# Performance work log

Hardware: AMD Instinct MI355X
Metric: run time of the kernel (lower is better)

Reference implementation:

```python
import jax, jax.numpy as jnp
from jax import lax
import numpy as np

DIM = 256


def setup_inputs() -> dict:
    key = jax.random.key(0)
    ks = jax.random.split(key, 7)
    B, C, H, W = 16, DIM, 64, 64
    s = 0.02
    return {
        "x": jax.random.normal(ks[0], (B, C, H, W), dtype=jnp.float32),
        "qkv_w": jax.random.normal(ks[1], (3 * C, C), dtype=jnp.float32) * s,
        "qkv_b": jnp.zeros((3 * C,), dtype=jnp.float32),
        "proj_w": jax.random.normal(ks[2], (C, C), dtype=jnp.float32) * s,
        "proj_b": jnp.zeros((C,), dtype=jnp.float32),
        "conv_w": jax.random.normal(ks[3], (C, C, 3, 3), dtype=jnp.float32) * s,
        "conv_b": jnp.zeros((C,), dtype=jnp.float32),
    }


def reference(x, qkv_w, qkv_b, proj_w, proj_b, conv_w, conv_b):
    B, C, H, W = x.shape
    N = H * W
    scale = C ** (-0.5)
    # qkv on channels-last tokens: [B,N,3C]
    xp = x.transpose(0, 2, 3, 1).reshape(B, N, C)
    qkv = xp @ qkv_w.T + qkv_b
    q, k, v = jnp.split(qkv, 3, axis=-1)  # each [B,N,C]
    q = q.transpose(0, 2, 1)  # [B,C,N]
    v = v.transpose(0, 2, 1)  # [B,C,N]
    # channel attention: [B,C,C]
    attn = jax.nn.softmax(jnp.einsum('bcn,bnd->bcd', q, k) * scale, axis=-1)
    out = jnp.einsum('bcd,bdn->bcn', attn, v).transpose(0, 2, 1)  # [B,N,C]
    out = out @ proj_w.T + proj_b  # [B,N,C]
    # faithful to original: direct reshape [B,N,C] -> [B,C,H,W]
    attn_out = out.reshape(B, C, H, W)
    conv_out = lax.conv_general_dilated(
        x, conv_w, window_strides=(1, 1), padding=[(1, 1), (1, 1)],
        dimension_numbers=('NCHW', 'OIHW', 'NCHW'))
    conv_out = conv_out + conv_b[None, :, None, None]
    return attn_out + conv_out
```

## Files before the change

kernel.cpp:

```cpp
#include <hip/hip_runtime.h>
#include <hip/hip_bf16.h>

typedef unsigned short u16;
typedef __bf16 bf16x8 __attribute__((ext_vector_type(8)));
typedef float f32x4 __attribute__((ext_vector_type(4)));

#define BATCH 16
#define C 256
#define NTOK 4096
#define CN 1048576

__device__ __forceinline__ u16 f2b(float f) {
  __hip_bfloat16 h = __float2bfloat16(f);
  return __builtin_bit_cast(u16, h);
}
__device__ __forceinline__ float b2f(u16 u) {
  unsigned int x = ((unsigned int)u) << 16;
  return __builtin_bit_cast(float, x);
}

__device__ __forceinline__ void glds16(const u16* g, u16* l) {
  __builtin_amdgcn_global_load_lds(
      (const __attribute__((address_space(1))) unsigned int*)(g),
      (__attribute__((address_space(3))) unsigned int*)(l), 16, 0, 0);
}

__global__ __launch_bounds__(256) void prep_x_kernel(
    const float* __restrict__ x, u16* __restrict__ xbf, u16* __restrict__ xT,
    float* __restrict__ rws) {
  __shared__ float t[32][33];
  int b = blockIdx.z;
  int c0 = blockIdx.y * 32, n0 = blockIdx.x * 32;
  int tid = threadIdx.x;
  int i = tid >> 3, j4 = (tid & 7) * 4;
  const float* xb = x + (long)b * CN;
  float4 v = *(const float4*)(xb + (long)(c0 + i) * NTOK + n0 + j4);
  ushort4 bv;
  bv.x = f2b(v.x); bv.y = f2b(v.y); bv.z = f2b(v.z); bv.w = f2b(v.w);
  *(ushort4*)(xbf + (long)b * CN + (long)(c0 + i) * NTOK + n0 + j4) = bv;
  t[i][j4 + 0] = v.x; t[i][j4 + 1] = v.y; t[i][j4 + 2] = v.z; t[i][j4 + 3] = v.w;
  __syncthreads();
  ushort4 o;
  o.x = f2b(t[j4 + 0][i]); o.y = f2b(t[j4 + 1][i]);
  o.z = f2b(t[j4 + 2][i]); o.w = f2b(t[j4 + 3][i]);
  *(ushort4*)(xT + (long)b * CN + (long)(n0 + i) * C + c0 + j4) = o;
  if (tid < 32) {
    float s = 0.f;
#pragma unroll
    for (int j = 0; j < 32; ++j) s += t[tid][j];
    atomicAdd(&rws[b * C + c0 + tid], s);
  }
}

__global__ __launch_bounds__(256) void prep_w_kernel(
    const float* __restrict__ qkv_w, const float* __restrict__ proj_w,
    const float* __restrict__ conv_w, u16* __restrict__ Wq, u16* __restrict__ Wk,
    u16* __restrict__ WvT, u16* __restrict__ Pw, u16* __restrict__ cw,
    float* __restrict__ rws, u16* __restrict__ zbuf) {
  int idx = blockIdx.x * 256 + threadIdx.x;
  if (idx < 4096) rws[idx] = 0.f;
  if (idx < 256) zbuf[idx] = 0;
  if (idx < 65536) {
    Wq[idx] = f2b(qkv_w[idx]);
  } else if (idx < 131072) {
    int e = idx - 65536;
    Wk[e] = f2b(qkv_w[65536 + e]);
  } else if (idx < 196608) {
    int e = idx - 131072;
    int i = e >> 8, d = e & 255;
    WvT[e] = f2b(qkv_w[131072 + d * 256 + i]);
  } else if (idx < 262144) {
    int e = idx - 196608;
    Pw[e] = f2b(proj_w[e]);
  } else if (idx < 851968) {
    int e = idx - 262144;
    int o = e / 2304;
    int rem = e - o * 2304;
    int tap = rem >> 8, i = rem & 255;
    cw[e] = f2b(conv_w[o * 2304 + i * 9 + tap]);
  }
}

__global__ __launch_bounds__(512) void bias_uw_kernel(
    const float* __restrict__ qkv_w, const float* __restrict__ r,
    float* __restrict__ u, float* __restrict__ w) {
  int b = blockIdx.x, t = threadIdx.x;
  const float* rb = r + b * C;
  if (t < 256) {
    float s = 0.f;
    for (int i = 0; i < C; ++i) s += qkv_w[(256 + t) * 256 + i] * rb[i];
    u[b * C + t] = s;
  } else {
    int c = t - 256;
    float s = 0.f;
    for (int i = 0; i < C; ++i) s += qkv_w[c * 256 + i] * rb[i];
    w[b * C + c] = s;
  }
}

template <int EPI>
__global__ __launch_bounds__(256, 2) void gemm_glds_kernel(
    const u16* __restrict__ A, const u16* __restrict__ B, void* __restrict__ Cv,
    int K, int lda, int ldb, int ldc, int tilesN, long sA, long sB, long sC,
    float scale, const float* __restrict__ e1, const float* __restrict__ e2,
    const float* __restrict__ e3, const float* __restrict__ e4, int e34stride) {
  int b = blockIdx.z, ks = blockIdx.y;
  A += (long)b * sA + (long)ks * K;
  B += (long)b * sB + (long)ks * K;
  int ty = blockIdx.x / tilesN, tx = blockIdx.x % tilesN;
  int row0 = ty * 128, col0 = tx * 128;

  __shared__ u16 lA[2][4096];
  __shared__ u16 lB[2][4096];

  int tid = threadIdx.x;
  int lane = tid & 63, wv = tid >> 6;
  int wm = wv >> 1, wn = wv & 1;
  int fr = lane & 15, kq = lane >> 4;
  int kqs = kq ^ ((fr >> 1) & 3);

  int c0 = wv * 128 + lane, c1 = c0 + 64;
  int r0s = c0 >> 2, r1s = c1 >> 2;
  int ls0 = (c0 & 3) ^ ((r0s >> 1) & 3);
  int ls1 = (c1 & 3) ^ ((r1s >> 1) & 3);
  const u16* pA0 = A + (long)(row0 + r0s) * lda + ls0 * 8;
  const u16* pA1 = A + (long)(row0 + r1s) * lda + ls1 * 8;
  const u16* pB0 = B + (long)(col0 + r0s) * ldb + ls0 * 8;
  const u16* pB1 = B + (long)(col0 + r1s) * ldb + ls1 * 8;
  int dst0 = wv * 1024, dst1 = wv * 1024 + 512;

  f32x4 acc[4][4] = {};

  auto STAGE = [&](int buf, int t) {
    int k0 = t << 5;
    glds16(pA0 + k0, &lA[buf][dst0]);
    glds16(pA1 + k0, &lA[buf][dst1]);
    glds16(pB0 + k0, &lB[buf][dst0]);
    glds16(pB1 + k0, &lB[buf][dst1]);
  };
  auto COMPUTE = [&](int buf) {
    bf16x8 af[4], bfr[4];
#pragma unroll
    for (int m = 0; m < 4; ++m)
      af[m] = *(const bf16x8*)&lA[buf][(wm * 64 + m * 16 + fr) * 32 + kqs * 8];
#pragma unroll
    for (int n = 0; n < 4; ++n)
      bfr[n] = *(const bf16x8*)&lB[buf][(wn * 64 + n * 16 + fr) * 32 + kqs * 8];
#pragma unroll
    for (int m = 0; m < 4; ++m)
#pragma unroll
      for (int n = 0; n < 4; ++n)
        acc[m][n] = __builtin_amdgcn_mfma_f32_16x16x32_bf16(af[m], bfr[n], acc[m][n], 0, 0, 0);
  };

  int nk = K >> 5, cur = 0;
  STAGE(0, 0);
  __syncthreads();
  for (int t = 0; t < nk; ++t) {
    if (t + 1 < nk) STAGE(cur ^ 1, t + 1);
    COMPUTE(cur);
    __syncthreads();
    cur ^= 1;
  }

  if (EPI == 0) {
    float* Cb = (float*)Cv + ((long)b * gridDim.y + ks) * sC;
#pragma unroll
    for (int m = 0; m < 4; ++m)
#pragma unroll
      for (int n = 0; n < 4; ++n)
#pragma unroll
        for (int r = 0; r < 4; ++r) {
          int gr = row0 + wm * 64 + m * 16 + kq * 4 + r;
          int gc = col0 + wn * 64 + n * 16 + fr;
          Cb[(long)gr * ldc + gc] = acc[m][n][r];
        }
  } else if (EPI == 1) {
    __hip_bfloat16* Cb = (__hip_bfloat16*)Cv + (long)b * sC;
#pragma unroll
    for (int m = 0; m < 4; ++m)
#pragma unroll
      for (int n = 0; n < 4; ++n)
#pragma unroll
        for (int r = 0; r < 4; ++r) {
          int gr = row0 + wm * 64 + m * 16 + kq * 4 + r;
          int gc = col0 + wn * 64 + n * 16 + fr;
          Cb[(long)gr * ldc + gc] = __float2bfloat16(acc[m][n][r]);
        }
  } else if (EPI == 2) {
    float* Cb = (float*)Cv + (long)b * sC;
    const float* ub = e3 + (long)b * e34stride;
    const float* wb = e4 + (long)b * e34stride;
#pragma unroll
    for (int m = 0; m < 4; ++m)
#pragma unroll
      for (int n = 0; n < 4; ++n)
#pragma unroll
        for (int r = 0; r < 4; ++r) {
          int gr = row0 + wm * 64 + m * 16 + kq * 4 + r;
          int gc = col0 + wn * 64 + n * 16 + fr;
          float v = acc[m][n][r] + e1[gr] * ub[gc] + e2[gc] * wb[gr] +
                    4096.0f * e1[gr] * e2[gc];
          Cb[(long)gr * ldc + gc] = v * scale;
        }
  }
}

__global__ __launch_bounds__(256) void reduceG_kernel(
    const float* __restrict__ Gp, u16* __restrict__ G) {
  int b = blockIdx.y;
  int e = blockIdx.x * 1024 + threadIdx.x * 4;
  const float* base = Gp + (long)b * 262144;
  float4 s = *(const float4*)(base + e);
#pragma unroll
  for (int sl = 1; sl < 4; ++sl) {
    float4 v = *(const float4*)(base + sl * 65536 + e);
    s.x += v.x; s.y += v.y; s.z += v.z; s.w += v.w;
  }
  ushort4 o;
  o.x = f2b(s.x); o.y = f2b(s.y); o.z = f2b(s.z); o.w = f2b(s.w);
  *(ushort4*)(G + (long)b * 65536 + e) = o;
}

__global__ __launch_bounds__(256) void softmax_kernel(const float* __restrict__ S,
                                                      u16* __restrict__ attnT) {
  int row = blockIdx.x;
  int t = threadIdx.x;
  float v = S[(long)row * C + t];
  __shared__ float red[256];
  red[t] = v; __syncthreads();
  for (int st = 128; st > 0; st >>= 1) {
    if (t < st) red[t] = fmaxf(red[t], red[t + st]);
    __syncthreads();
  }
  float mx = red[0];
  __syncthreads();
  float e = __expf(v - mx);
  red[t] = e; __syncthreads();
  for (int st = 128; st > 0; st >>= 1) {
    if (t < st) red[t] += red[t + st];
    __syncthreads();
  }
  float inv = 1.0f / red[0];
  int b = row >> 8, c = row & 255;
  attnT[(long)b * 65536 + t * 256 + c] = f2b(e * inv);
}

__global__ __launch_bounds__(256) void cbias_kernel(const u16* __restrict__ M,
                                                    const float* __restrict__ qkv_b,
                                                    const float* __restrict__ proj_b,
                                                    float* __restrict__ cb) {
  int b = blockIdx.x, j = threadIdx.x;
  const u16* m = M + (long)b * 65536 + (long)j * 256;
  float s = 0.f;
  for (int d = 0; d < C; ++d) s += b2f(m[d]) * qkv_b[512 + d];
  cb[b * C + j] = proj_b[j] + s;
}

__global__ __launch_bounds__(256, 2) void convattn_kernel(
    const u16* __restrict__ xT, const u16* __restrict__ cw,
    const u16* __restrict__ W2, const u16* __restrict__ zbuf,
    const float* __restrict__ conv_b, const float* __restrict__ cb,
    float* __restrict__ out) {
  int b = blockIdx.y;
  int to = blockIdx.x >> 5;
  int tn = blockIdx.x & 31;
  int row0 = to * 128, col0 = tn * 128;
  const u16* xTb = xT + (long)b * CN;
  const u16* W2b = W2 + (long)b * 65536;

  __shared__ u16 lA[2][8192];
  __shared__ u16 lB[2][8192];

  int tid = threadIdx.x;
  int lane = tid & 63, w = tid >> 6;
  int wm = w >> 1, wn = w & 1;
  int fr = lane & 15, kq = lane >> 4;
  int fx = fr & 7;

  int lr = lane >> 3, sl = lane & 7;
  int ss = sl ^ lr;

  const u16* aA[4]; const u16* pBt[4]; int hh[4], ww[4];
  const u16* zsrc = zbuf + ss * 8;
#pragma unroll
  for (int i = 0; i < 4; ++i) {
    int r = w * 32 + i * 8 + lr;
    aA[i] = cw + (long)(row0 + r) * 2304 + ss * 8;
    int t = col0 + r;
    hh[i] = t >> 6; ww[i] = t & 63;
    pBt[i] = xTb + (long)t * 256 + ss * 8;
  }
  int nb = col0 >> 8, jb = col0 & 255;

  f32x4 acc[4][4] = {};
  const u16 *at0, *at1, *at2, *at3, *bt0, *bt1, *bt2, *bt3;

  auto set_tap = [&](int tap) {
    int dh = tap / 3 - 1, dw = tap % 3 - 1;
    long sh = (long)(dh * 64 + dw) * 256;
    at0 = aA[0] + tap * 256; at1 = aA[1] + tap * 256;
    at2 = aA[2] + tap * 256; at3 = aA[3] + tap * 256;
    bool v0 = ((unsigned)(hh[0] + dh) < 64u) && ((unsigned)(ww[0] + dw) < 64u);
    bool v1 = ((unsigned)(hh[1] + dh) < 64u) && ((unsigned)(ww[1] + dw) < 64u);
    bool v2 = ((unsigned)(hh[2] + dh) < 64u) && ((unsigned)(ww[2] + dw) < 64u);
    bool v3 = ((unsigned)(hh[3] + dh) < 64u) && ((unsigned)(ww[3] + dw) < 64u);
    bt0 = v0 ? pBt[0] + sh : zsrc;
    bt1 = v1 ? pBt[1] + sh : zsrc;
    bt2 = v2 ? pBt[2] + sh : zsrc;
    bt3 = v3 ? pBt[3] + sh : zsrc;
  };
  auto set_attn = [&]() {
#pragma unroll
    for (int i = 0; i < 4; ++i) {
      int r = w * 32 + i * 8 + lr;
      const u16* a = xTb + (long)((row0 + r) * 16 + nb) * 256 + ss * 8;
      const u16* bb = W2b + (long)(jb + r) * 256 + ss * 8;
      if (i == 0) { at0 = a; bt0 = bb; }
      else if (i == 1) { at1 = a; bt1 = bb; }
      else if (i == 2) { at2 = a; bt2 = bb; }
      else { at3 = a; bt3 = bb; }
    }
  };

  auto STAGE = [&](int buf, int chunk) {
    int k = chunk * 64;
    glds16(at0 + k, &lA[buf][(w * 32 + 0) * 64]);
    glds16(at1 + k, &lA[buf][(w * 32 + 8) * 64]);
    glds16(at2 + k, &lA[buf][(w * 32 + 16) * 64]);
    glds16(at3 + k, &lA[buf][(w * 32 + 24) * 64]);
    glds16(bt0 + k, &lB[buf][(w * 32 + 0) * 64]);
    glds16(bt1 + k, &lB[buf][(w * 32 + 8) * 64]);
    glds16(bt2 + k, &lB[buf][(w * 32 + 16) * 64]);
    glds16(bt3 + k, &lB[buf][(w * 32 + 24) * 64]);
  };
  auto COMPUTE = [&](int buf) {
    bf16x8 af[4][2], bf[4][2];
#pragma unroll
    for (int m = 0; m < 4; ++m) {
      int row = wm * 64 + m * 16 + fr;
#pragma unroll
      for (int kh = 0; kh < 2; ++kh)
        af[m][kh] = *(const bf16x8*)&lA[buf][row * 64 + (((kh << 2) + kq) ^ fx) * 8];
    }
#pragma unroll
    for (int n = 0; n < 4; ++n) {
      int row = wn * 64 + n * 16 + fr;
#pragma unroll
      for (int kh = 0; kh < 2; ++kh)
        bf[n][kh] = *(const bf16x8*)&lB[buf][row * 64 + (((kh << 2) + kq) ^ fx) * 8];
    }
    __builtin_amdgcn_s_setprio(1);
#pragma unroll
    for (int kh = 0; kh < 2; ++kh)
#pragma unroll
      for (int m = 0; m < 4; ++m)
#pragma unroll
        for (int n = 0; n < 4; ++n)
          acc[m][n] = __builtin_amdgcn_mfma_f32_16x16x32_bf16(af[m][kh], bf[n][kh], acc[m][n], 0, 0, 0);
    __builtin_amdgcn_s_setprio(0);
  };

  set_tap(0);
  STAGE(0, 0);
  asm volatile("s_waitcnt vmcnt(0)" ::: "memory");
  __builtin_amdgcn_sched_barrier(0);
  __builtin_amdgcn_s_barrier();
  __builtin_amdgcn_sched_barrier(0);

  int buf = 0;
#pragma unroll 1
  for (int T = 0; T < 10; ++T) {
#pragma unroll
    for (int j = 0; j < 4; ++j) {
      if (!(T == 9 && j == 3)) {
        if (j < 3) {
          STAGE(buf ^ 1, j + 1);
        } else {
          if (T < 8) set_tap(T + 1);
          else set_attn();
          STAGE(buf ^ 1, 0);
        }
      }
      COMPUTE(buf);
      asm volatile("s_waitcnt vmcnt(0)" ::: "memory");
      __builtin_amdgcn_sched_barrier(0);
      __builtin_amdgcn_s_barrier();
      __builtin_amdgcn_sched_barrier(0);
      buf ^= 1;
    }
  }

  float* ob = out + (long)b * CN;
  const float* cbb = cb + b * C;
#pragma unroll
  for (int m = 0; m < 4; ++m) {
    int go = row0 + wm * 64 + m * 16 + kq * 4;
#pragma unroll
    for (int nn = 0; nn < 4; ++nn) {
      int cc = wn * 64 + nn * 16 + fr;
      float cbv = cbb[jb + cc];
#pragma unroll
      for (int r = 0; r < 4; ++r)
        ob[(long)(go + r) * NTOK + col0 + cc] =
            acc[m][nn][r] + conv_b[go + r] + cbv;
    }
  }
}

extern "C" void kernel_launch(void* const* d_in, const int* in_sizes, int n_in,
                              void* d_out, int out_size, void* d_ws, size_t ws_size,
                              hipStream_t stream) {
  const float* x = (const float*)d_in[0];
  const float* qkv_w = (const float*)d_in[1];
  const float* qkv_b = (const float*)d_in[2];
  const float* proj_w = (const float*)d_in[3];
  const float* proj_b = (const float*)d_in[4];
  const float* conv_w = (const float*)d_in[5];
  const float* conv_b = (const float*)d_in[6];
  float* out = (float*)d_out;
  char* ws = (char*)d_ws;

  u16* xbf = (u16*)(ws);
  u16* xT = (u16*)(ws + 33554432);
  u16* Gbf = (u16*)(ws + 67108864);
  float* Gpart = (float*)(ws + 69206016);
  u16* T1bf = (u16*)(ws + 69206016);
  float* Sf = (float*)(ws + 71303168);
  u16* attnT = (u16*)(ws + 75497472);
  u16* Mbf = (u16*)(ws + 77594624);
  u16* W2bf = (u16*)(ws + 79691776);
  u16* Wq = (u16*)(ws + 85983232);
  u16* Wk = (u16*)(ws + 86114304);
  u16* WvT = (u16*)(ws + 86245376);
  u16* Pw = (u16*)(ws + 86376448);
  u16* cw = (u16*)(ws + 86507520);
  float* rws = (float*)(ws + 87687168);
  float* uws = (float*)(ws + 87703552);
  float* wws = (float*)(ws + 87719936);
  float* cb = (float*)(ws + 87736320);
  u16* zbuf = (u16*)(ws + 87752704);

  prep_w_kernel<<<3328, 256, 0, stream>>>(qkv_w, proj_w, conv_w, Wq, Wk, WvT,
                                          Pw, cw, rws, zbuf);
  prep_x_kernel<<<dim3(128, 8, BATCH), 256, 0, stream>>>(x, xbf, xT, rws);
  bias_uw_kernel<<<BATCH, 512, 0, stream>>>(qkv_w, rws, uws, wws);

  gemm_glds_kernel<0><<<dim3(4, 4, BATCH), 256, 0, stream>>>(
      xbf, xbf, Gpart, 1024, 4096, 4096, 256, 2, CN, CN, 65536,
      0.f, nullptr, nullptr, nullptr, nullptr, 0);
  reduceG_kernel<<<dim3(64, BATCH), 256, 0, stream>>>(Gpart, Gbf);

  gemm_glds_kernel<1><<<dim3(4, 1, BATCH), 256, 0, stream>>>(
      Wq, Gbf, T1bf, 256, 256, 256, 256, 2, 0, 65536, 65536,
      0.f, nullptr, nullptr, nullptr, nullptr, 0);
  gemm_glds_kernel<2><<<dim3(4, 1, BATCH), 256, 0, stream>>>(
      T1bf, Wk, Sf, 256, 256, 256, 256, 2, 65536, 0, 65536,
      0.0625f, qkv_b, qkv_b + 256, uws, wws, 256);

  softmax_kernel<<<BATCH * C, 256, 0, stream>>>(Sf, attnT);

  gemm_glds_kernel<1><<<dim3(4, 1, BATCH), 256, 0, stream>>>(
      Pw, attnT, Mbf, 256, 256, 256, 256, 2, 0, 65536, 65536,
      0.f, nullptr, nullptr, nullptr, nullptr, 0);
  cbias_kernel<<<BATCH, 256, 0, stream>>>(Mbf, qkv_b, proj_b, cb);
  gemm_glds_kernel<1><<<dim3(4, 1, BATCH), 256, 0, stream>>>(
      Mbf, WvT, W2bf, 256, 256, 256, 256, 2, 65536, 0, 65536,
      0.f, nullptr, nullptr, nullptr, nullptr, 0);

  convattn_kernel<<<dim3(64, BATCH), 256, 0, stream>>>(xT, cw, W2bf, zbuf,
                                                       conv_b, cb, out);
}
```

Baseline: 218.6 us.

## Load A operand directly from global into registers, dropping A LDS staging

The conv-weight and attention A-operand tiles are now read by each lane straight from global memory into double-buffered registers in MFMA fragment layout, instead of being staged through shared memory. This halves LDS use and removes the A-side LDS reads, which could raise occupancy and cut LDS traffic. In exchange each wave issues uncoalesced 16-byte global loads, and rows shared by two waves (wn=0/1) are fetched twice. Register pressure also grows from the two A register buffers.

```diff
diff --git a/kernel.cpp b/kernel.cpp
--- a/kernel.cpp
+++ b/kernel.cpp
@@ -269,7 +269,6 @@
   const u16* xTb = xT + (long)b * CN;
   const u16* W2b = W2 + (long)b * 65536;
 
-  __shared__ u16 lA[2][8192];
   __shared__ u16 lB[2][8192];
 
   int tid = threadIdx.x;
@@ -281,26 +280,31 @@
   int lr = lane >> 3, sl = lane & 7;
   int ss = sl ^ lr;
 
-  const u16* aA[4]; const u16* pBt[4]; int hh[4], ww[4];
+  const u16* pBt[4]; int hh[4], ww[4];
   const u16* zsrc = zbuf + ss * 8;
 #pragma unroll
   for (int i = 0; i < 4; ++i) {
-    int r = w * 32 + i * 8 + lr;
-    aA[i] = cw + (long)(row0 + r) * 2304 + ss * 8;
-    int t = col0 + r;
+    int t = col0 + w * 32 + i * 8 + lr;
     hh[i] = t >> 6; ww[i] = t & 63;
     pBt[i] = xTb + (long)t * 256 + ss * 8;
   }
   int nb = col0 >> 8, jb = col0 & 255;
 
+  const u16* aP[4];
+#pragma unroll
+  for (int m = 0; m < 4; ++m)
+    aP[m] = cw + (long)(row0 + wm * 64 + m * 16 + fr) * 2304 + kq * 8;
+  const u16* aQ[4];
+#pragma unroll
+  for (int m = 0; m < 4; ++m)
+    aQ[m] = xTb + (long)((row0 + wm * 64 + m * 16 + fr) * 16 + nb) * 256 + kq * 8;
+
   f32x4 acc[4][4] = {};
-  const u16 *at0, *at1, *at2, *at3, *bt0, *bt1, *bt2, *bt3;
-
-  auto set_tap = [&](int tap) {
+  const u16 *bt0, *bt1, *bt2, *bt3;
+
+  auto set_tapB = [&](int tap) {
     int dh = tap / 3 - 1, dw = tap % 3 - 1;
     long sh = (long)(dh * 64 + dw) * 256;
-    at0 = aA[0] + tap * 256; at1 = aA[1] + tap * 256;
-    at2 = aA[2] + tap * 256; at3 = aA[3] + tap * 256;
     bool v0 = ((unsigned)(hh[0] + dh) < 64u) && ((unsigned)(ww[0] + dw) < 64u);
     bool v1 = ((unsigned)(hh[1] + dh) < 64u) && ((unsigned)(ww[1] + dw) < 64u);
     bool v2 = ((unsigned)(hh[2] + dh) < 64u) && ((unsigned)(ww[2] + dw) < 64u);
@@ -310,45 +314,39 @@
     bt2 = v2 ? pBt[2] + sh : zsrc;
     bt3 = v3 ? pBt[3] + sh : zsrc;
   };
-  auto set_attn = [&]() {
-#pragma unroll
-    for (int i = 0; i < 4; ++i) {
-      int r = w * 32 + i * 8 + lr;
-      const u16* a = xTb + (long)((row0 + r) * 16 + nb) * 256 + ss * 8;
-      const u16* bb = W2b + (long)(jb + r) * 256 + ss * 8;
-      if (i == 0) { at0 = a; bt0 = bb; }
-      else if (i == 1) { at1 = a; bt1 = bb; }
-      else if (i == 2) { at2 = a; bt2 = bb; }
-      else { at3 = a; bt3 = bb; }
-    }
-  };
-
-  auto STAGE = [&](int buf, int chunk) {
+  auto set_attnB = [&]() {
+    bt0 = W2b + (long)(jb + w * 32 + 0 + lr) * 256 + ss * 8;
+    bt1 = W2b + (long)(jb + w * 32 + 8 + lr) * 256 + ss * 8;
+    bt2 = W2b + (long)(jb + w * 32 + 16 + lr) * 256 + ss * 8;
+    bt3 = W2b + (long)(jb + w * 32 + 24 + lr) * 256 + ss * 8;
+  };
+
+  auto STAGE_B = [&](int buf, int chunk) {
     int k = chunk * 64;
-    glds16(at0 + k, &lA[buf][(w * 32 + 0) * 64]);
-    glds16(at1 + k, &lA[buf][(w * 32 + 8) * 64]);
-    glds16(at2 + k, &lA[buf][(w * 32 + 16) * 64]);
-    glds16(at3 + k, &lA[buf][(w * 32 + 24) * 64]);
     glds16(bt0 + k, &lB[buf][(w * 32 + 0) * 64]);
     glds16(bt1 + k, &lB[buf][(w * 32 + 8) * 64]);
     glds16(bt2 + k, &lB[buf][(w * 32 + 16) * 64]);
     glds16(bt3 + k, &lB[buf][(w * 32 + 24) * 64]);
   };
-  auto COMPUTE = [&](int buf) {
-    bf16x8 af[4][2], bf[4][2];
+
+  bf16x8 aR0[4][2], aR1[4][2];
+  auto LOADA = [&](bf16x8 (&d)[4][2]) {
 #pragma unroll
     for (int m = 0; m < 4; ++m) {
-      int row = wm * 64 + m * 16 + fr;
-#pragma unroll
-      for (int kh = 0; kh < 2; ++kh)
-        af[m][kh] = *(const bf16x8*)&lA[buf][row * 64 + (((kh << 2) + kq) ^ fx) * 8];
+      d[m][0] = *(const bf16x8*)(aP[m]);
+      d[m][1] = *(const bf16x8*)(aP[m] + 32);
     }
+#pragma unroll
+    for (int m = 0; m < 4; ++m) aP[m] += 64;
+  };
+  auto COMPUTE = [&](int buf, const bf16x8 (&a)[4][2]) {
+    bf16x8 bf_[4][2];
 #pragma unroll
     for (int n = 0; n < 4; ++n) {
       int row = wn * 64 + n * 16 + fr;
 #pragma unroll
       for (int kh = 0; kh < 2; ++kh)
-        bf[n][kh] = *(const bf16x8*)&lB[buf][row * 64 + (((kh << 2) + kq) ^ fx) * 8];
+        bf_[n][kh] = *(const bf16x8*)&lB[buf][row * 64 + (((kh << 2) + kq) ^ fx) * 8];
     }
     __builtin_amdgcn_s_setprio(1);
 #pragma unroll
@@ -357,12 +355,13 @@
       for (int m = 0; m < 4; ++m)
 #pragma unroll
         for (int n = 0; n < 4; ++n)
-          acc[m][n] = __builtin_amdgcn_mfma_f32_16x16x32_bf16(af[m][kh], bf[n][kh], acc[m][n], 0, 0, 0);
+          acc[m][n] = __builtin_amdgcn_mfma_f32_16x16x32_bf16(a[m][kh], bf_[n][kh], acc[m][n], 0, 0, 0);
     __builtin_amdgcn_s_setprio(0);
   };
 
-  set_tap(0);
-  STAGE(0, 0);
+  set_tapB(0);
+  STAGE_B(0, 0);
+  LOADA(aR0);
   asm volatile("s_waitcnt vmcnt(0)" ::: "memory");
   __builtin_amdgcn_sched_barrier(0);
   __builtin_amdgcn_s_barrier();
@@ -373,16 +372,20 @@
   for (int T = 0; T < 10; ++T) {
 #pragma unroll
     for (int j = 0; j < 4; ++j) {
-      if (!(T == 9 && j == 3)) {
-        if (j < 3) {
-          STAGE(buf ^ 1, j + 1);
-        } else {
-          if (T < 8) set_tap(T + 1);
-          else set_attn();
-          STAGE(buf ^ 1, 0);
+      bool last = (T == 9) && (j == 3);
+      if (!last) {
+        if (j == 3) {
+          if (T < 8) set_tapB(T + 1);
+          else set_attnB();
+          if (T == 8) {
+#pragma unroll
+            for (int m = 0; m < 4; ++m) aP[m] = aQ[m];
+          }
         }
+        if ((j & 1) == 0) LOADA(aR1); else LOADA(aR0);
+        STAGE_B(buf ^ 1, (j < 3) ? j + 1 : 0);
       }
-      COMPUTE(buf);
+      if ((j & 1) == 0) COMPUTE(buf, aR0); else COMPUTE(buf, aR1);
       asm volatile("s_waitcnt vmcnt(0)" ::: "memory");
       __builtin_amdgcn_sched_barrier(0);
       __builtin_amdgcn_s_barrier();
```

Measured after the change: 309.7 us. +41.7%, slower.
